# Kernel tuning notes

Measured on AMD Instinct MI355X. Metric: run time of the kernel, lower is better.

The kernel has to match this reference:

```python
import jax, jax.numpy as jnp
import numpy as np


def setup_inputs() -> dict:
    key = jax.random.key(0)
    k1, k2 = jax.random.split(key)
    BATCH, NUM_PROBES, DIM = 2048, 512, 256
    X = jax.random.uniform(k1, (BATCH, DIM), dtype=jnp.float32)
    probes = jax.random.uniform(k2, (NUM_PROBES, DIM), dtype=jnp.float32)
    return {"X": X, "probes": probes}


def reference(X, probes):
    # Godel implication a -> b: 1.0 if a <= b else b, applied on the
    # broadcast [batch, num_probes, dim] grid, then mean over dim.
    Xe = X[:, None, :]            # [B, 1, D]
    Pe = probes[None, :, :]       # [1, P, D]
    implication = jnp.where(Pe <= Xe, jnp.float32(1.0), Xe)  # [B, P, D]
    return implication.mean(axis=-1)  # [B, P]
```

## Files before the change

### kernel.cpp

```cpp
#include <hip/hip_runtime.h>
#include <stdint.h>


#define BATCH  2048
#define NPROBE 512
#define DIM    256

typedef float f4 __attribute__((ext_vector_type(4)));

static __device__ __forceinline__ void gl_lds16(const void* g, void* l) {
  __builtin_amdgcn_global_load_lds(
      (const __attribute__((address_space(1))) void*)g,
      (__attribute__((address_space(3))) void*)l, 16, 0, 0);
}

__global__ __launch_bounds__(1024, 4)
void yoneda_kernel(const float* __restrict__ X, const float* __restrict__ Pr,
                   float* __restrict__ out) {
  __shared__ float lds[32768];
  float* Xs = lds;
  float* Ps = lds + 16384;

  const int tid = threadIdx.x;
  const int b0 = blockIdx.y * 64, p0 = blockIdx.x * 64;
  const float K  =  16777216.0f;
  const float mK = -16777216.0f;

  #pragma unroll
  for (int s = 0; s < 4; ++s) {
    int idx = s * 1024 + tid;
    int r = idx >> 6, q = idx & 63;
    int qs = q ^ (r & 7);
    gl_lds16(X + (size_t)(b0 + r) * DIM + 4 * qs, &Xs[idx * 4]);
  }
  #pragma unroll
  for (int s = 0; s < 4; ++s) {
    int idx = s * 1024 + tid;
    int r = idx >> 6, q = idx & 63;
    int qs = q ^ (r & 7);
    f4 v = *(const f4*)(Pr + (size_t)(p0 + r) * DIM + 4 * qs);
    f4 t;
    #pragma unroll
    for (int e = 0; e < 4; ++e) t[e] = __builtin_fmaf(v[e], mK, 1.0f);
    *(f4*)&Ps[idx * 4] = t;
  }

  const int g    = tid >> 7;
  const int gtid = tid & 127;
  const int tb   = gtid >> 3;
  const int tp   = gtid & 7;

  int xb[4], pb[8];
  #pragma unroll
  for (int i = 0; i < 4; ++i)
    xb[i] = (tb + 16 * i) * 1024 + g * 128 + 16 * (tb & 7);
  #pragma unroll
  for (int j = 0; j < 8; ++j)
    pb[j] = 65536 + (tp + 8 * j) * 1024 + g * 128 + 16 * tp;

  float acc[4][8];
  float accx[4];
  #pragma unroll
  for (int i = 0; i < 4; ++i) {
    accx[i] = 0.0f;
    #pragma unroll
    for (int j = 0; j < 8; ++j) acc[i][j] = 0.0f;
  }

  __syncthreads();

  #pragma unroll
  for (int s = 0; s < 8; ++s) {
    f4 xv[4], pv[8];
    #pragma unroll
    for (int i = 0; i < 4; ++i)
      xv[i] = *(const f4*)((const char*)lds + (xb[i] ^ (16 * s)));
    #pragma unroll
    for (int j = 0; j < 8; ++j)
      pv[j] = *(const f4*)((const char*)lds + (pb[j] ^ (16 * s)));

    #pragma unroll
    for (int i = 0; i < 4; ++i)
      #pragma unroll
      for (int e = 0; e < 4; ++e) {
        float x = xv[i][e];
        float y = 1.0f - x;
        accx[i] += x;
        #pragma unroll
        for (int j = 0; j < 8; ++j) {
          float m;
          asm("v_fma_f32 %0, %1, %2, %3 clamp"
              : "=v"(m) : "v"(x), "v"(K), "v"(pv[j][e]));
          acc[i][j] = __builtin_fmaf(m, y, acc[i][j]);
        }
      }
  }

  __syncthreads();
  float* cbuf = lds;
  if (g > 0) {
    #pragma unroll
    for (int i = 0; i < 4; ++i)
      #pragma unroll
      for (int j = 0; j < 8; ++j) {
        int e = i * 8 + j;
        cbuf[(e * 7 + (g - 1)) * 128 + gtid] = acc[i][j] + accx[i];
      }
  }
  __syncthreads();
  if (g == 0) {
    const float inv = 1.0f / 256.0f;
    #pragma unroll
    for (int i = 0; i < 4; ++i) {
      size_t ro = (size_t)(b0 + tb + 16 * i) * NPROBE + p0 + tp;
      #pragma unroll
      for (int j = 0; j < 8; ++j) {
        int e = i * 8 + j;
        float v = acc[i][j] + accx[i];
        #pragma unroll
        for (int k = 0; k < 7; ++k)
          v += cbuf[(e * 7 + k) * 128 + gtid];
        out[ro + 8 * j] = v * inv;
      }
    }
  }
}

extern "C" void kernel_launch(void* const* d_in, const int* in_sizes, int n_in,
                              void* d_out, int out_size, void* d_ws, size_t ws_size,
                              hipStream_t stream) {
  const float* X  = (const float*)d_in[0];
  const float* Pr = (const float*)d_in[1];
  float* out = (float*)d_out;
  dim3 grid(NPROBE / 64, BATCH / 64);
  yoneda_kernel<<<grid, 1024, 0, stream>>>(X, Pr, out);
}
```

Before: 23.57 us.

## Halve block size with 8x8 per-thread tiles and parallel swizzled reduction

Blocks drop from 1024 to 512 threads, and each thread now computes an 8x8 register tile instead of 4x8, so every LDS-loaded X value is reused across more probes. The cross-group reduction becomes vectorized f4 writes into an XOR-swizzled buffer, with all threads sharing the final summation instead of only group 0. The aim is to cut LDS traffic per FMA and remove the serialized reduction tail. In exchange there is higher register pressure and fewer waves per block, which could lower latency hiding.

```diff
diff --git a/kernel.cpp b/kernel.cpp
--- a/kernel.cpp
+++ b/kernel.cpp
@@ -14,7 +14,7 @@
       (__attribute__((address_space(3))) void*)l, 16, 0, 0);
 }
 
-__global__ __launch_bounds__(1024, 4)
+__global__ __launch_bounds__(512, 2)
 void yoneda_kernel(const float* __restrict__ X, const float* __restrict__ Pr,
                    float* __restrict__ out) {
   __shared__ float lds[32768];
@@ -27,15 +27,15 @@
   const float mK = -16777216.0f;
 
   #pragma unroll
-  for (int s = 0; s < 4; ++s) {
-    int idx = s * 1024 + tid;
+  for (int s = 0; s < 8; ++s) {
+    int idx = s * 512 + tid;
     int r = idx >> 6, q = idx & 63;
     int qs = q ^ (r & 7);
     gl_lds16(X + (size_t)(b0 + r) * DIM + 4 * qs, &Xs[idx * 4]);
   }
   #pragma unroll
-  for (int s = 0; s < 4; ++s) {
-    int idx = s * 1024 + tid;
+  for (int s = 0; s < 8; ++s) {
+    int idx = s * 512 + tid;
     int r = idx >> 6, q = idx & 63;
     int qs = q ^ (r & 7);
     f4 v = *(const f4*)(Pr + (size_t)(p0 + r) * DIM + 4 * qs);
@@ -45,23 +45,22 @@
     *(f4*)&Ps[idx * 4] = t;
   }
 
-  const int g    = tid >> 7;
-  const int gtid = tid & 127;
+  const int g    = tid >> 6;
+  const int gtid = tid & 63;
   const int tb   = gtid >> 3;
   const int tp   = gtid & 7;
 
-  int xb[4], pb[8];
+  int xb[8], pb[8];
   #pragma unroll
-  for (int i = 0; i < 4; ++i)
-    xb[i] = (tb + 16 * i) * 1024 + g * 128 + 16 * (tb & 7);
+  for (int i = 0; i < 8; ++i) {
+    xb[i] = (tb + 8 * i) * 1024 + g * 128 + 16 * tb;
+    pb[i] = 65536 + (tp + 8 * i) * 1024 + g * 128 + 16 * tp;
+  }
+
+  float acc[8][8];
+  float accx[8];
   #pragma unroll
-  for (int j = 0; j < 8; ++j)
-    pb[j] = 65536 + (tp + 8 * j) * 1024 + g * 128 + 16 * tp;
-
-  float acc[4][8];
-  float accx[4];
-  #pragma unroll
-  for (int i = 0; i < 4; ++i) {
+  for (int i = 0; i < 8; ++i) {
     accx[i] = 0.0f;
     #pragma unroll
     for (int j = 0; j < 8; ++j) acc[i][j] = 0.0f;
@@ -71,16 +70,16 @@
 
   #pragma unroll
   for (int s = 0; s < 8; ++s) {
-    f4 xv[4], pv[8];
+    f4 xv[8], pv[8];
     #pragma unroll
-    for (int i = 0; i < 4; ++i)
+    for (int i = 0; i < 8; ++i)
       xv[i] = *(const f4*)((const char*)lds + (xb[i] ^ (16 * s)));
     #pragma unroll
     for (int j = 0; j < 8; ++j)
       pv[j] = *(const f4*)((const char*)lds + (pb[j] ^ (16 * s)));
 
     #pragma unroll
-    for (int i = 0; i < 4; ++i)
+    for (int i = 0; i < 8; ++i)
       #pragma unroll
       for (int e = 0; e < 4; ++e) {
         float x = xv[i][e];
@@ -97,32 +96,34 @@
   }
 
   __syncthreads();
-  float* cbuf = lds;
-  if (g > 0) {
+  f4* cbuf = (f4*)lds;
+  #pragma unroll
+  for (int i = 0; i < 8; ++i)
     #pragma unroll
-    for (int i = 0; i < 4; ++i)
+    for (int j4 = 0; j4 < 2; ++j4) {
+      int c = (i * 2 + j4) * 64 + gtid;
+      f4 v;
       #pragma unroll
-      for (int j = 0; j < 8; ++j) {
-        int e = i * 8 + j;
-        cbuf[(e * 7 + (g - 1)) * 128 + gtid] = acc[i][j] + accx[i];
-      }
-  }
+      for (int k = 0; k < 4; ++k) v[k] = acc[i][4 * j4 + k] + accx[i];
+      cbuf[c * 8 + (g ^ (c & 7))] = v;
+    }
   __syncthreads();
-  if (g == 0) {
-    const float inv = 1.0f / 256.0f;
+  const float inv = 1.0f / 256.0f;
+  #pragma unroll
+  for (int cc = 0; cc < 2; ++cc) {
+    int c  = tid + cc * 512;
+    int sw = c & 7;
+    f4 v = cbuf[c * 8 + sw];
     #pragma unroll
-    for (int i = 0; i < 4; ++i) {
-      size_t ro = (size_t)(b0 + tb + 16 * i) * NPROBE + p0 + tp;
-      #pragma unroll
-      for (int j = 0; j < 8; ++j) {
-        int e = i * 8 + j;
-        float v = acc[i][j] + accx[i];
-        #pragma unroll
-        for (int k = 0; k < 7; ++k)
-          v += cbuf[(e * 7 + k) * 128 + gtid];
-        out[ro + 8 * j] = v * inv;
-      }
-    }
+    for (int g2 = 1; g2 < 8; ++g2)
+      v += cbuf[c * 8 + (g2 ^ sw)];
+    int gt2 = c & 63, ij = c >> 6;
+    int i2 = ij >> 1, j4 = ij & 1;
+    int row = b0 + (gt2 >> 3) + 8 * i2;
+    int col = p0 + (gt2 & 7) + 32 * j4;
+    #pragma unroll
+    for (int k = 0; k < 4; ++k)
+      out[(size_t)row * NPROBE + col + 8 * k] = v[k] * inv;
   }
 }
 
@@ -133,5 +134,5 @@
   const float* Pr = (const float*)d_in[1];
   float* out = (float*)d_out;
   dim3 grid(NPROBE / 64, BATCH / 64);
-  yoneda_kernel<<<grid, 1024, 0, stream>>>(X, Pr, out);
+  yoneda_kernel<<<grid, 512, 0, stream>>>(X, Pr, out);
 }
```

After: 22.34 us. -5.2%, faster.
